# Performance work log

Hardware: AMD Instinct MI355X
Metric: run time of the kernel (lower is better)

The kernel has to match this reference:

```python
import jax, jax.numpy as jnp
import numpy as np

IN_OCT = 512
OUT_OCT = 512
BATCH = 512


def setup_inputs() -> dict:
    key = jax.random.key(0)
    kx, kw = jax.random.split(key)
    x = jax.random.normal(kx, (BATCH, IN_OCT * 8), dtype=jnp.float32)
    weight = jax.random.normal(kw, (OUT_OCT, IN_OCT, 8, 8), dtype=jnp.float32)
    bias = jnp.zeros((OUT_OCT, 8), dtype=jnp.float32)
    return {"x": x, "weight": weight, "bias": bias}


def reference(x, weight, bias):
    # x: [B, in_oct*8]; weight: [out_oct, in_oct, 8, 8]; bias: [out_oct, 8]
    B = x.shape[0]
    out_oct, in_oct = weight.shape[0], weight.shape[1]
    xo = x.reshape(B, in_oct, 8)
    # octonion_mul(x[:, j], weight[i, j]) applies the per-pair 8x8 octonion
    # left-multiplication matrix; summed over j it is one bilinear contraction.
    y = jnp.einsum("bjp,ijpk->bik", xo, weight) + bias[None, :, :]
    return y.reshape(B, out_oct * 8)
```

## Files before the change

kernel.cpp:

```cpp
#include <hip/hip_runtime.h>
#include <stdint.h>


#define M_DIM 512
#define N_DIM 4096
#define K_DIM 4096
#define KSPLIT 4
#define NIT ((K_DIM / KSPLIT) / 32)
#define PART_ELEMS (M_DIM * N_DIM)

typedef __bf16 bf16x8 __attribute__((ext_vector_type(8)));
typedef float f32x4 __attribute__((ext_vector_type(4)));

__device__ inline unsigned short f2bf(float f) {
  union { float f; unsigned int u; } v;
  v.f = f;
  unsigned int u = v.u;
  unsigned int r = (u + 0x7fffu + ((u >> 16) & 1u)) >> 16;
  return (unsigned short)r;
}

__global__ __launch_bounds__(256) void prep_kernel(
    const float* __restrict__ x, const float* __restrict__ w,
    const float* __restrict__ bias, unsigned short* __restrict__ abf,
    unsigned short* __restrict__ bt, float* __restrict__ out) {
  const int bid = blockIdx.x;
  const int t = threadIdx.x;
  if (bid < 4096) {
    __shared__ __align__(16) unsigned short lT[8][512];
    const int i = bid >> 3;
    const int jg = bid & 7;
    const float4* src =
        (const float4*)(w + (size_t)i * 32768 + jg * 4096 + t * 16);
    float4 v0 = src[0], v1 = src[1], v2 = src[2], v3 = src[3];
    const int jp = (t >> 2) * 8 + (t & 3) * 2;
    const float* lo = (const float*)&v0;
    const float* hi = (const float*)&v2;
#pragma unroll
    for (int k = 0; k < 4; ++k) {
      unsigned int pk =
          (unsigned int)f2bf(lo[k]) | ((unsigned int)f2bf(hi[k]) << 16);
      *(unsigned int*)&lT[k][jp] = pk;
    }
    lo = (const float*)&v1;
    hi = (const float*)&v3;
#pragma unroll
    for (int k = 0; k < 4; ++k) {
      unsigned int pk =
          (unsigned int)f2bf(lo[k]) | ((unsigned int)f2bf(hi[k]) << 16);
      *(unsigned int*)&lT[k + 4][jp] = pk;
    }
    __syncthreads();
    const int r = t >> 5, c = t & 31;
    const uint4* s = (const uint4*)&lT[r][c * 16];
    uint4* d = (uint4*)(bt + (size_t)(i * 8 + r) * K_DIM + jg * 512 + c * 16);
    d[0] = s[0];
    d[1] = s[1];
  } else if (bid < 5120) {
    int g = (bid - 4096) * 256 + t;
    const float4* xi = (const float4*)x;
    float4 a = xi[g * 2];
    float4 b = xi[g * 2 + 1];
    __attribute__((aligned(16))) unsigned short o[8] = {
        f2bf(a.x), f2bf(a.y), f2bf(a.z), f2bf(a.w),
        f2bf(b.x), f2bf(b.y), f2bf(b.z), f2bf(b.w)};
    *(uint4*)(abf + (size_t)g * 8) = *(const uint4*)o;
  } else {
    int g = (bid - 5120) * 256 + t;
    int el = g * 4;
    int col = el & (N_DIM - 1);
    *(float4*)(out + el) = *(const float4*)(bias + col);
  }
}

__device__ inline void gld16(const void* g, void* l) {
  __builtin_amdgcn_global_load_lds(
      (const __attribute__((address_space(1))) unsigned int*)g,
      (__attribute__((address_space(3))) unsigned int*)l, 16, 0, 0);
}

__global__ __launch_bounds__(512, 4) void gemm_kernel(
    const unsigned short* __restrict__ A, const unsigned short* __restrict__ Bt,
    float* __restrict__ out, float* __restrict__ part, int use_atomic) {
  __shared__ __align__(16) char lds[2][16 * 1024];
  const int t = threadIdx.x;
  const int n0 = blockIdx.x * 128;
  const int m0 = blockIdx.y * 128;
  const int z = blockIdx.z;
  const int kc0 = z * (K_DIM / KSPLIT);
  const int w = t >> 6;
  const int lane = t & 63;
  const int wr = w >> 2;
  const int wc = w & 3;
  const int lrow = lane & 15;
  const int kb = lane >> 4;

  f32x4 acc[4][2] = {};

  const size_t aOff = (size_t)(m0 + (t >> 2)) * K_DIM + kc0 + (t & 3) * 8;
  const size_t bOff = (size_t)(n0 + (t >> 2)) * K_DIM + kc0 + (t & 3) * 8;

  auto issue = [&](int it) {
    char* buf = lds[it & 1];
    gld16(A + aOff + it * 32, buf + t * 16);
    gld16(Bt + bOff + it * 32, buf + 8192 + t * 16);
  };

  issue(0);
  for (int it = 0; it < NIT; ++it) {
    __syncthreads();
    if (it + 1 < NIT) issue(it + 1);
    const unsigned short* cA = (const unsigned short*)lds[it & 1];
    const unsigned short* cB = cA + 4096;

    bf16x8 af[4], bfr[2];
#pragma unroll
    for (int mt = 0; mt < 4; ++mt)
      af[mt] = *(const bf16x8*)(cA + (wr * 64 + mt * 16 + lrow) * 32 + kb * 8);
#pragma unroll
    for (int nt = 0; nt < 2; ++nt)
      bfr[nt] = *(const bf16x8*)(cB + (wc * 32 + nt * 16 + lrow) * 32 + kb * 8);
#pragma unroll
    for (int mt = 0; mt < 4; ++mt)
#pragma unroll
      for (int nt = 0; nt < 2; ++nt)
        acc[mt][nt] = __builtin_amdgcn_mfma_f32_16x16x32_bf16(
            af[mt], bfr[nt], acc[mt][nt], 0, 0, 0);
  }

#pragma unroll
  for (int mt = 0; mt < 4; ++mt) {
    const int gmb = m0 + wr * 64 + mt * 16 + kb * 4;
#pragma unroll
    for (int nt = 0; nt < 2; ++nt) {
      const int gn = n0 + wc * 32 + nt * 16 + lrow;
      if (use_atomic) {
#pragma unroll
        for (int r = 0; r < 4; ++r)
          atomicAdd(out + (size_t)(gmb + r) * N_DIM + gn, acc[mt][nt][r]);
      } else {
        float* p = part + (size_t)z * PART_ELEMS;
#pragma unroll
        for (int r = 0; r < 4; ++r)
          p[(size_t)(gmb + r) * N_DIM + gn] = acc[mt][nt][r];
      }
    }
  }
}

__global__ __launch_bounds__(256) void reduce_kernel(
    const float* __restrict__ part, const float* __restrict__ bias,
    float* __restrict__ out) {
  const int g = blockIdx.x * 256 + threadIdx.x;
  const float4* p = (const float4*)part;
  const float4* b4 = (const float4*)bias;
  const int Q = PART_ELEMS / 4;
  float4 s0 = p[g];
  float4 s1 = p[g + Q];
  float4 s2 = p[g + 2 * Q];
  float4 s3 = p[g + 3 * Q];
  float4 bb = b4[g & (N_DIM / 4 - 1)];
  float4 r;
  r.x = s0.x + s1.x + s2.x + s3.x + bb.x;
  r.y = s0.y + s1.y + s2.y + s3.y + bb.y;
  r.z = s0.z + s1.z + s2.z + s3.z + bb.z;
  r.w = s0.w + s1.w + s2.w + s3.w + bb.w;
  ((float4*)out)[g] = r;
}

extern "C" void kernel_launch(void* const* d_in, const int* in_sizes, int n_in,
                              void* d_out, int out_size, void* d_ws,
                              size_t ws_size, hipStream_t stream) {
  const float* x = (const float*)d_in[0];
  const float* w = (const float*)d_in[1];
  const float* bias = (const float*)d_in[2];
  float* out = (float*)d_out;

  unsigned short* abf = (unsigned short*)d_ws;
  unsigned short* bt = abf + (size_t)M_DIM * K_DIM;
  float* part = (float*)((char*)d_ws + 36u * 1024 * 1024);

  const bool have_ws = ws_size >= 68ull * 1024 * 1024;
  const int use_atomic = have_ws ? 0 : 1;

  prep_kernel<<<use_atomic ? 7168 : 5120, 256, 0, stream>>>(x, w, bias, abf,
                                                            bt, out);

  dim3 grid(N_DIM / 128, M_DIM / 128, KSPLIT);
  gemm_kernel<<<grid, 512, 0, stream>>>(abf, bt, out, part, use_atomic);

  if (!use_atomic)
    reduce_kernel<<<PART_ELEMS / 4 / 256, 256, 0, stream>>>(part, bias, out);
}
```

Before: 139.1 us.

## Replace split-K GEMM and reduce pass with 64x64-tile full-K GEMM

Drops the 4-way split-K scheme, which wrote four fp32 partial outputs and then ran a separate reduce kernel. Each GEMM block now computes a 64x64 output tile over the full K range with 256 threads and adds the bias in the epilogue. This removes the partial-buffer round trip (about 32 MB of writes and reads) and one kernel launch. In exchange each block runs a four times longer serial K loop with less data reuse per tile, though the grid stays at 512 blocks.

```diff
diff --git a/kernel.cpp b/kernel.cpp
--- a/kernel.cpp
+++ b/kernel.cpp
@@ -5,9 +5,7 @@
 #define M_DIM 512
 #define N_DIM 4096
 #define K_DIM 4096
-#define KSPLIT 4
-#define NIT ((K_DIM / KSPLIT) / 32)
-#define PART_ELEMS (M_DIM * N_DIM)
+#define NIT (K_DIM / 32)
 
 typedef __bf16 bf16x8 __attribute__((ext_vector_type(8)));
 typedef float f32x4 __attribute__((ext_vector_type(4)));
@@ -22,8 +20,7 @@
 
 __global__ __launch_bounds__(256) void prep_kernel(
     const float* __restrict__ x, const float* __restrict__ w,
-    const float* __restrict__ bias, unsigned short* __restrict__ abf,
-    unsigned short* __restrict__ bt, float* __restrict__ out) {
+    unsigned short* __restrict__ abf, unsigned short* __restrict__ bt) {
   const int bid = blockIdx.x;
   const int t = threadIdx.x;
   if (bid < 4096) {
@@ -56,7 +53,7 @@
     uint4* d = (uint4*)(bt + (size_t)(i * 8 + r) * K_DIM + jg * 512 + c * 16);
     d[0] = s[0];
     d[1] = s[1];
-  } else if (bid < 5120) {
+  } else {
     int g = (bid - 4096) * 256 + t;
     const float4* xi = (const float4*)x;
     float4 a = xi[g * 2];
@@ -65,11 +62,6 @@
         f2bf(a.x), f2bf(a.y), f2bf(a.z), f2bf(a.w),
         f2bf(b.x), f2bf(b.y), f2bf(b.z), f2bf(b.w)};
     *(uint4*)(abf + (size_t)g * 8) = *(const uint4*)o;
-  } else {
-    int g = (bid - 5120) * 256 + t;
-    int el = g * 4;
-    int col = el & (N_DIM - 1);
-    *(float4*)(out + el) = *(const float4*)(bias + col);
   }
 }
 
@@ -79,31 +71,31 @@
       (__attribute__((address_space(3))) unsigned int*)l, 16, 0, 0);
 }
 
-__global__ __launch_bounds__(512, 4) void gemm_kernel(
+__global__ __launch_bounds__(256) void gemm_kernel(
     const unsigned short* __restrict__ A, const unsigned short* __restrict__ Bt,
-    float* __restrict__ out, float* __restrict__ part, int use_atomic) {
-  __shared__ __align__(16) char lds[2][16 * 1024];
+    const float* __restrict__ bias, float* __restrict__ out) {
+  __shared__ __align__(16) char lds[2][8 * 1024];
   const int t = threadIdx.x;
-  const int n0 = blockIdx.x * 128;
-  const int m0 = blockIdx.y * 128;
-  const int z = blockIdx.z;
-  const int kc0 = z * (K_DIM / KSPLIT);
+  const int n0 = blockIdx.x * 64;
+  const int m0 = blockIdx.y * 64;
   const int w = t >> 6;
   const int lane = t & 63;
-  const int wr = w >> 2;
-  const int wc = w & 3;
+  const int wr = w >> 1;
+  const int wc = w & 1;
   const int lrow = lane & 15;
   const int kb = lane >> 4;
 
-  f32x4 acc[4][2] = {};
+  f32x4 acc[2][2] = {};
 
-  const size_t aOff = (size_t)(m0 + (t >> 2)) * K_DIM + kc0 + (t & 3) * 8;
-  const size_t bOff = (size_t)(n0 + (t >> 2)) * K_DIM + kc0 + (t & 3) * 8;
+  const int srow = t >> 2;
+  const int scol = (t & 3) * 8;
+  const size_t aOff = (size_t)(m0 + srow) * K_DIM + scol;
+  const size_t bOff = (size_t)(n0 + srow) * K_DIM + scol;
 
   auto issue = [&](int it) {
     char* buf = lds[it & 1];
     gld16(A + aOff + it * 32, buf + t * 16);
-    gld16(Bt + bOff + it * 32, buf + 8192 + t * 16);
+    gld16(Bt + bOff + it * 32, buf + 4096 + t * 16);
   };
 
   issue(0);
@@ -111,17 +103,17 @@
     __syncthreads();
     if (it + 1 < NIT) issue(it + 1);
     const unsigned short* cA = (const unsigned short*)lds[it & 1];
-    const unsigned short* cB = cA + 4096;
+    const unsigned short* cB = cA + 2048;
 
-    bf16x8 af[4], bfr[2];
+    bf16x8 af[2], bfr[2];
 #pragma unroll
-    for (int mt = 0; mt < 4; ++mt)
-      af[mt] = *(const bf16x8*)(cA + (wr * 64 + mt * 16 + lrow) * 32 + kb * 8);
+    for (int mt = 0; mt < 2; ++mt)
+      af[mt] = *(const bf16x8*)(cA + (wr * 32 + mt * 16 + lrow) * 32 + kb * 8);
 #pragma unroll
     for (int nt = 0; nt < 2; ++nt)
       bfr[nt] = *(const bf16x8*)(cB + (wc * 32 + nt * 16 + lrow) * 32 + kb * 8);
 #pragma unroll
-    for (int mt = 0; mt < 4; ++mt)
+    for (int mt = 0; mt < 2; ++mt)
 #pragma unroll
       for (int nt = 0; nt < 2; ++nt)
         acc[mt][nt] = __builtin_amdgcn_mfma_f32_16x16x32_bf16(
@@ -129,43 +121,17 @@
   }
 
 #pragma unroll
-  for (int mt = 0; mt < 4; ++mt) {
-    const int gmb = m0 + wr * 64 + mt * 16 + kb * 4;
+  for (int mt = 0; mt < 2; ++mt) {
+    const int gmb = m0 + wr * 32 + mt * 16 + kb * 4;
 #pragma unroll
     for (int nt = 0; nt < 2; ++nt) {
       const int gn = n0 + wc * 32 + nt * 16 + lrow;
-      if (use_atomic) {
+      const float bv = bias[gn];
 #pragma unroll
-        for (int r = 0; r < 4; ++r)
-          atomicAdd(out + (size_t)(gmb + r) * N_DIM + gn, acc[mt][nt][r]);
-      } else {
-        float* p = part + (size_t)z * PART_ELEMS;
-#pragma unroll
-        for (int r = 0; r < 4; ++r)
-          p[(size_t)(gmb + r) * N_DIM + gn] = acc[mt][nt][r];
-      }
+      for (int r = 0; r < 4; ++r)
+        out[(size_t)(gmb + r) * N_DIM + gn] = acc[mt][nt][r] + bv;
     }
   }
-}
-
-__global__ __launch_bounds__(256) void reduce_kernel(
-    const float* __restrict__ part, const float* __restrict__ bias,
-    float* __restrict__ out) {
-  const int g = blockIdx.x * 256 + threadIdx.x;
-  const float4* p = (const float4*)part;
-  const float4* b4 = (const float4*)bias;
-  const int Q = PART_ELEMS / 4;
-  float4 s0 = p[g];
-  float4 s1 = p[g + Q];
-  float4 s2 = p[g + 2 * Q];
-  float4 s3 = p[g + 3 * Q];
-  float4 bb = b4[g & (N_DIM / 4 - 1)];
-  float4 r;
-  r.x = s0.x + s1.x + s2.x + s3.x + bb.x;
-  r.y = s0.y + s1.y + s2.y + s3.y + bb.y;
-  r.z = s0.z + s1.z + s2.z + s3.z + bb.z;
-  r.w = s0.w + s1.w + s2.w + s3.w + bb.w;
-  ((float4*)out)[g] = r;
 }
 
 extern "C" void kernel_launch(void* const* d_in, const int* in_sizes, int n_in,
@@ -178,17 +144,10 @@
 
   unsigned short* abf = (unsigned short*)d_ws;
   unsigned short* bt = abf + (size_t)M_DIM * K_DIM;
-  float* part = (float*)((char*)d_ws + 36u * 1024 * 1024);
+  (void)ws_size;
 
-  const bool have_ws = ws_size >= 68ull * 1024 * 1024;
-  const int use_atomic = have_ws ? 0 : 1;
+  prep_kernel<<<5120, 256, 0, stream>>>(x, w, abf, bt);
 
-  prep_kernel<<<use_atomic ? 7168 : 5120, 256, 0, stream>>>(x, w, bias, abf,
-                                                            bt, out);
-
-  dim3 grid(N_DIM / 128, M_DIM / 128, KSPLIT);
-  gemm_kernel<<<grid, 512, 0, stream>>>(abf, bt, out, part, use_atomic);
-
-  if (!use_atomic)
-    reduce_kernel<<<PART_ELEMS / 4 / 256, 256, 0, stream>>>(part, bias, out);
+  dim3 grid(N_DIM / 64, M_DIM / 64);
+  gemm_kernel<<<grid, 256, 0, stream>>>(abf, bt, bias, out);
 }
```

Result: slower. 143.7 us (+3.3%).
